# Optimization experiments

Measured on AMD Instinct MI355X. Metric: run time of the kernel, lower is better.

The kernel has to match this reference:

```python
import jax, jax.numpy as jnp
import numpy as np

IMG_H, IMG_W = 256, 704  # full image shape (img_metas['img_shape'])
EPS = 1e-5
B, N_CAM, D_REF, C_CH = 1, 6, 1, 256
HF, WF = 32, 88
DD = 64
BEV_H = BEV_W = 128
Q = BEV_H * BEV_W


def inverse_sigmoid(x, eps=1e-5):
    x = jnp.clip(x, 0.0, 1.0)
    return jnp.log(jnp.clip(x, eps) / jnp.clip(1.0 - x, eps))


def grid_sample_2d(feat, grid):
    # feat [N,C,H,W], grid [N,Hg,Wg,2] (x,y in [-1,1]); bilinear, zeros padding, align_corners=False
    Nn, C, H, W = feat.shape
    x = (grid[..., 0] + 1.0) * 0.5 * W - 0.5
    y = (grid[..., 1] + 1.0) * 0.5 * H - 0.5
    x0 = jnp.floor(x)
    y0 = jnp.floor(y)
    wx = x - x0
    wy = y - y0
    x0 = x0.astype(jnp.int32)
    y0 = y0.astype(jnp.int32)

    def gather(ix, iy):
        valid = (ix >= 0) & (ix < W) & (iy >= 0) & (iy < H)
        ixc = jnp.clip(ix, 0, W - 1)
        iyc = jnp.clip(iy, 0, H - 1)
        v = jax.vmap(lambda f, jx, jy: f[:, jy, jx])(feat, ixc, iyc)  # [N,C,Hg,Wg]
        return v * valid[:, None].astype(feat.dtype)

    return (gather(x0, y0) * ((1 - wx) * (1 - wy))[:, None]
            + gather(x0 + 1, y0) * (wx * (1 - wy))[:, None]
            + gather(x0, y0 + 1) * ((1 - wx) * wy)[:, None]
            + gather(x0 + 1, y0 + 1) * (wx * wy)[:, None])


def grid_sample_3d(vol, grid):
    # vol [N,C,D,H,W], grid [N,Dg,Hg,Wg,3] (x,y,z); trilinear, zeros padding, align_corners=False
    Nn, C, D, H, W = vol.shape
    x = (grid[..., 0] + 1.0) * 0.5 * W - 0.5
    y = (grid[..., 1] + 1.0) * 0.5 * H - 0.5
    z = (grid[..., 2] + 1.0) * 0.5 * D - 0.5
    x0 = jnp.floor(x); y0 = jnp.floor(y); z0 = jnp.floor(z)
    wx = x - x0; wy = y - y0; wz = z - z0
    x0 = x0.astype(jnp.int32); y0 = y0.astype(jnp.int32); z0 = z0.astype(jnp.int32)

    def gather(ix, iy, iz):
        valid = (ix >= 0) & (ix < W) & (iy >= 0) & (iy < H) & (iz >= 0) & (iz < D)
        ixc = jnp.clip(ix, 0, W - 1)
        iyc = jnp.clip(iy, 0, H - 1)
        izc = jnp.clip(iz, 0, D - 1)
        v = jax.vmap(lambda f, jx, jy, jz: f[:, jz, jy, jx])(vol, ixc, iyc, izc)
        return v * valid[:, None].astype(vol.dtype)

    return (gather(x0, y0, z0) * ((1 - wx) * (1 - wy) * (1 - wz))[:, None]
            + gather(x0 + 1, y0, z0) * (wx * (1 - wy) * (1 - wz))[:, None]
            + gather(x0, y0 + 1, z0) * ((1 - wx) * wy * (1 - wz))[:, None]
            + gather(x0 + 1, y0 + 1, z0) * (wx * wy * (1 - wz))[:, None]
            + gather(x0, y0, z0 + 1) * ((1 - wx) * (1 - wy) * wz)[:, None]
            + gather(x0 + 1, y0, z0 + 1) * (wx * (1 - wy) * wz)[:, None]
            + gather(x0, y0 + 1, z0 + 1) * ((1 - wx) * wy * wz)[:, None]
            + gather(x0 + 1, y0 + 1, z0 + 1) * (wx * wy * wz)[:, None])


def setup_inputs() -> dict:
    key = jax.random.key(0)
    ks = jax.random.split(key, 12)
    feat = jax.random.normal(ks[0], (B * N_CAM, C_CH, HF, WF), jnp.float32)
    bev_queries = jax.random.normal(ks[1], (B, Q, C_CH), jnp.float32)
    bev_pos = jax.random.normal(ks[2], (B, Q, C_CH), jnp.float32)
    reference_points = jax.random.uniform(ks[3], (B, D_REF, Q, 3), jnp.float32)
    pc_range = jnp.array([-51.2, -51.2, -5.0, 51.2, 51.2, 3.0], jnp.float32)
    # semi-realistic lidar->image projection matrices: intrinsics * axis-swap * yaw per camera
    f, cx, cy = 500.0, IMG_W / 2.0, IMG_H / 2.0
    K = np.array([[f, 0, cx, 0], [0, f, cy, 0], [0, 0, 1, 0], [0, 0, 0, 1]], np.float32)
    A = np.array([[0, -1, 0, 0], [0, 0, -1, 0], [1, 0, 0, 0], [0, 0, 0, 1]], np.float32)
    mats = []
    for i in range(N_CAM):
        th = 2.0 * np.pi * i / N_CAM
        c, s = np.cos(th), np.sin(th)
        R = np.array([[c, s, 0, 0], [-s, c, 0, 0], [0, 0, 1, 0], [0, 0, 0, 1]], np.float32)
        mats.append(K @ A @ R)
    lidar_to_img = jnp.asarray(np.stack(mats))[None]  # [1,N,4,4]
    depth_prob = jax.random.uniform(ks[4], (B * N_CAM, DD, HF, WF), jnp.float32)
    sc = 0.02
    return {
        'feat': feat, 'bev_queries': bev_queries, 'bev_pos': bev_pos,
        'reference_points': reference_points, 'pc_range': pc_range,
        'lidar_to_img': lidar_to_img, 'depth_prob': depth_prob,
        'w_pos': jax.random.normal(ks[5], (C_CH, 1), jnp.float32) * sc,
        'b_pos': jnp.zeros((1,), jnp.float32),
        'w_img': jax.random.normal(ks[6], (C_CH, N_CAM * 2), jnp.float32) * sc,
        'b_img': jnp.zeros((N_CAM * 2,), jnp.float32),
        'w_att': jax.random.normal(ks[7], (C_CH, N_CAM), jnp.float32) * sc,
        'b_att': jnp.zeros((N_CAM,), jnp.float32),
        'conv_w': jax.random.normal(ks[8], (C_CH, C_CH, 3, 3), jnp.float32) * sc,
        'conv_b': jnp.zeros((C_CH,), jnp.float32),
        'bn_gamma': jnp.ones((C_CH,), jnp.float32),
        'bn_beta': jnp.zeros((C_CH,), jnp.float32),
        'bn_mean': jnp.zeros((C_CH,), jnp.float32),
        'bn_var': jnp.ones((C_CH,), jnp.float32),
        'se_w': jax.random.normal(ks[9], (C_CH, C_CH), jnp.float32) * sc,
        'se_b': jnp.zeros((C_CH,), jnp.float32),
        'cbam_w': jax.random.normal(ks[10], (1, 2, 7, 7), jnp.float32) * 0.05,
        'cbam_b': jnp.zeros((1,), jnp.float32),
        'bev_h': BEV_H, 'bev_w': BEV_W,
    }


def reference(feat, bev_queries, bev_pos, reference_points, pc_range, lidar_to_img, depth_prob,
              w_pos, b_pos, w_img, b_img, w_att, b_att, conv_w, conv_b,
              bn_gamma, bn_beta, bn_mean, bn_var, se_w, se_b, cbam_w, cbam_b, bev_h, bev_w):
    Bq, Qn = bev_queries.shape[:2]
    D = reference_points.shape[1]
    N = lidar_to_img.shape[1]
    BN, C, Hf, Wf = feat.shape
    q = bev_queries + bev_pos
    pos_offset = q @ w_pos + b_pos  # [B,Q,1] (only_use_height)
    z = jax.nn.sigmoid(inverse_sigmoid(reference_points[..., 2:3]) + pos_offset[:, None])
    rp = jnp.concatenate([reference_points[..., :2], z], axis=-1)  # [B,D,Q,3]
    attn = (q @ w_att + b_att).reshape(Bq, 1, Qn, N, 1)
    img_off = q @ w_img + b_img  # [B,Q,2N]
    # unnormalize to lidar coords; apply_3d_transformation == identity (no aug)
    pts = rp * (pc_range[3:] - pc_range[:3]) + pc_range[:3]
    pts4 = jnp.concatenate([pts, jnp.ones_like(pts[..., :1])], axis=-1)  # [B,D,Q,4]
    cam = jnp.einsum('bnij,bdqj->dbnqi', lidar_to_img, pts4)  # [D,B,N,Q,4]
    ref_depth = cam[..., 2:3]
    mask = ref_depth > EPS
    xy = cam[..., :2] / jnp.maximum(cam[..., 2:3], EPS)
    xy = xy / jnp.array([IMG_W, IMG_H], dtype=xy.dtype)
    xy = (xy - 0.5) * 2.0
    mask = mask & (xy[..., 0:1] > -1.0) & (xy[..., 0:1] < 1.0) & (xy[..., 1:2] > -1.0) & (xy[..., 1:2] < 1.0)
    Dd = depth_prob.shape[1]
    ref_depth = (ref_depth / Dd - 0.5) * 2.0
    mask = mask & (ref_depth > -1.0) & (ref_depth < 1.0)
    bev_mask = jnp.transpose(mask, (1, 4, 3, 2, 0)).astype(feat.dtype)  # [B,1,Q,N,D]
    off = img_off.reshape(Bq, Qn, N, 2).transpose(0, 2, 1, 3)[None] / jnp.array([Wf, Hf], dtype=feat.dtype)
    xy = xy + off  # [D,B,N,Q,2]
    grid = xy.transpose(1, 2, 3, 0, 4).reshape(BN, Qn, D, 2)
    sampled = grid_sample_2d(feat, grid).reshape(Bq, N, C, Qn, D).transpose(0, 2, 3, 1, 4)  # [B,C,Q,N,D]
    grid3 = jnp.concatenate([xy, ref_depth], axis=-1).transpose(1, 2, 3, 0, 4).reshape(BN, 1, Qn, D, 3)
    dp = grid_sample_3d(depth_prob[:, None], grid3).reshape(Bq, N, 1, Qn, D).transpose(0, 2, 3, 1, 4)
    bev_mask = jnp.nan_to_num(dp) * bev_mask
    w = jax.nn.sigmoid(attn) * jnp.nan_to_num(bev_mask)
    agg = (jnp.nan_to_num(sampled) * w)[..., 0].sum(-1)  # [B,C,Q] (D==1)
    x = agg.reshape(Bq, C, bev_h, bev_w)
    dn = ('NCHW', 'OIHW', 'NCHW')
    x = jax.lax.conv_general_dilated(x, conv_w, (1, 1), ((1, 1), (1, 1)), dimension_numbers=dn) + conv_b[None, :, None, None]
    x = (x - bn_mean[None, :, None, None]) * (bn_gamma / jnp.sqrt(bn_var + 1e-5))[None, :, None, None] + bn_beta[None, :, None, None]
    x = jax.nn.relu(x)
    s = x.mean(axis=(2, 3))  # SE: global avg pool + 1x1 conv + sigmoid
    x = x * jax.nn.sigmoid(s @ se_w.T + se_b)[:, :, None, None]
    a = jnp.concatenate([x.max(axis=1, keepdims=True), x.mean(axis=1, keepdims=True)], axis=1)  # CBAM spatial
    a = jax.lax.conv_general_dilated(a, cbam_w, (1, 1), ((3, 3), (3, 3)), dimension_numbers=dn) + cbam_b[None, :, None, None]
    x = x * jax.nn.sigmoid(a)
    out = x.reshape(Bq, C, bev_h * bev_w).transpose(0, 2, 1)
    return out, rp
```

## Files before the change

kernel.cpp:

```cpp
#include <hip/hip_runtime.h>
#include <math.h>

#define QN   16384
#define CCH  256
#define NCAM 6
#define HFD  32
#define WFD  88
#define DDD  64
#define BEVH 128
#define BEVW 128
#define IMGW 704.0f
#define IMGH 256.0f
#define EPSV 1e-5f

typedef __attribute__((ext_vector_type(8))) short bf8_t;
typedef __attribute__((ext_vector_type(8))) unsigned short us8;
typedef __attribute__((ext_vector_type(4))) unsigned short us4;
typedef __attribute__((ext_vector_type(4))) float f4_t;

__device__ __forceinline__ float sigmoidf_(float x){ return 1.0f/(1.0f+__expf(-x)); }

__device__ __forceinline__ unsigned short f2bf(float f){
    unsigned int b = __float_as_uint(f);
    b += 0x7FFFu + ((b >> 16) & 1u);
    return (unsigned short)(b >> 16);
}
__device__ __forceinline__ float bf2f(unsigned short u){
    return __uint_as_float(((unsigned int)u) << 16);
}

__global__ __launch_bounds__(256) void k_prep(const float* __restrict__ feat, unsigned short* __restrict__ feat_tH,
                                              const float* __restrict__ cw, unsigned short* __restrict__ wtH,
                                              const float* __restrict__ se_w, float* __restrict__ se_wT,
                                              float* __restrict__ ssum){
    int b = blockIdx.x;
    if (b < 4224){
        __shared__ float tile[32][33];
        int n   = b / 704;
        int rem = b - n*704;
        int cb  = (rem / 88) * 32;
        int pb  = (rem % 88) * 32;
        int tx = threadIdx.x & 31, ty = threadIdx.x >> 5;
        for (int r = ty; r < 32; r += 8)
            tile[r][tx] = feat[(size_t)(n*256 + cb + r)*2816 + pb + tx];
        __syncthreads();
        for (int r = ty; r < 32; r += 8)
            feat_tH[(size_t)(n*2816 + pb + r)*256 + cb + tx] = f2bf(tile[tx][r]);
    } else if (b < 6528){
        int b2 = b - 4224;
        if (b2 == 0) ssum[threadIdx.x] = 0.f;
        int idx = b2*256 + threadIdx.x;
        int ci = idx & 255;
        int co = (idx >> 8) & 255;
        int kk = idx >> 16;
        int kh = kk/3, kw = kk - kh*3;
        int chunk = ci >> 6, ciin = ci & 63;
        size_t dst = ((((size_t)(kh*4 + chunk)*3 + kw)*256 + co) << 6) + ciin;
        wtH[dst] = f2bf(cw[(size_t)(co*256 + ci)*9 + kk]);
    } else {
        __shared__ float tile[32][33];
        int tb = b - 6528;
        int rb_ = (tb >> 3) * 32;
        int cb_ = (tb & 7) * 32;
        int tx = threadIdx.x & 31, ty = threadIdx.x >> 5;
        for (int r = ty; r < 32; r += 8)
            tile[r][tx] = se_w[(size_t)(rb_ + r)*256 + cb_ + tx];
        __syncthreads();
        for (int r = ty; r < 32; r += 8)
            se_wT[(size_t)(cb_ + r)*256 + rb_ + tx] = tile[tx][r];
    }
}

__global__ __launch_bounds__(256) void k_proj(
    const float* __restrict__ bq, const float* __restrict__ bpos,
    const float* __restrict__ refp,
    const float* __restrict__ w_pos, const float* __restrict__ b_pos,
    const float* __restrict__ w_img, const float* __restrict__ w_att,
    float* __restrict__ Sg, float* __restrict__ out_rp)
{
    __shared__ float wlf[19][260];
    __shared__ unsigned short Aq[64][264];
    __shared__ float sl[64][20];
    int tid = threadIdx.x;
    int lane = tid & 63, wid = tid >> 6;
    int l15 = lane & 15, quad = lane >> 4;
    int q0 = blockIdx.x * 64;

    wlf[0][tid] = w_pos[tid];
    #pragma unroll
    for (int r = 0; r < 6; r++){
        int idx = r*256 + tid;
        int c = idx / 6, j = idx - 6*c;
        wlf[1 + j][c] = w_att[idx];
    }
    #pragma unroll
    for (int r = 0; r < 12; r++){
        int idx = r*256 + tid;
        int c = idx / 12, j = idx - 12*c;
        wlf[7 + j][c] = w_img[idx];
    }
    #pragma unroll
    for (int r = 0; r < 16; r++){
        int row = r*4 + wid;
        int cc  = lane * 4;
        float4 a = *(const float4*)(bq   + (size_t)(q0+row)*CCH + cc);
        float4 b = *(const float4*)(bpos + (size_t)(q0+row)*CCH + cc);
        us4 o;
        o.x = f2bf(a.x+b.x); o.y = f2bf(a.y+b.y); o.z = f2bf(a.z+b.z); o.w = f2bf(a.w+b.w);
        *(us4*)&Aq[row][cc] = o;
    }
    __syncthreads();

    f4_t acc0 = (f4_t){0.f,0.f,0.f,0.f};
    f4_t acc1 = (f4_t){0.f,0.f,0.f,0.f};
    #pragma unroll
    for (int kc = 0; kc < 8; kc++){
        bf8_t af = *(bf8_t*)&Aq[wid*16 + l15][kc*32 + quad*8];
        bf8_t b0, b1;
        {
            const float* wr = &wlf[l15][kc*32 + quad*8];
            float4 w0 = *(const float4*)wr;
            float4 w1 = *(const float4*)(wr + 4);
            b0[0]=(short)f2bf(w0.x); b0[1]=(short)f2bf(w0.y); b0[2]=(short)f2bf(w0.z); b0[3]=(short)f2bf(w0.w);
            b0[4]=(short)f2bf(w1.x); b0[5]=(short)f2bf(w1.y); b0[6]=(short)f2bf(w1.z); b0[7]=(short)f2bf(w1.w);
        }
        if (l15 < 3){
            const float* wr = &wlf[16 + l15][kc*32 + quad*8];
            float4 w0 = *(const float4*)wr;
            float4 w1 = *(const float4*)(wr + 4);
            b1[0]=(short)f2bf(w0.x); b1[1]=(short)f2bf(w0.y); b1[2]=(short)f2bf(w0.z); b1[3]=(short)f2bf(w0.w);
            b1[4]=(short)f2bf(w1.x); b1[5]=(short)f2bf(w1.y); b1[6]=(short)f2bf(w1.z); b1[7]=(short)f2bf(w1.w);
        } else {
            b1 = (bf8_t){0,0,0,0,0,0,0,0};
        }
        acc0 = __builtin_amdgcn_mfma_f32_16x16x32_bf16(af, b0, acc0, 0, 0, 0);
        acc1 = __builtin_amdgcn_mfma_f32_16x16x32_bf16(af, b1, acc1, 0, 0, 0);
    }
    #pragma unroll
    for (int r = 0; r < 4; r++){
        int qq = wid*16 + quad*4 + r;
        sl[qq][l15] = acc0[r];
        if (l15 < 3) sl[qq][16 + l15] = acc1[r];
    }
    __syncthreads();

    if (tid < 64){
        int q = q0 + tid;
        float pos_off = sl[tid][0] + b_pos[0];
        float rx = refp[q*3+0], ry = refp[q*3+1], rz = refp[q*3+2];
        float zc_ = fminf(fmaxf(rz, 0.f), 1.f);
        float inv = logf(fmaxf(zc_, EPSV) / fmaxf(1.f - zc_, EPSV));
        float znew = sigmoidf_(inv + pos_off);
        out_rp[q*3+0] = rx; out_rp[q*3+1] = ry; out_rp[q*3+2] = znew;
        sl[tid][19] = znew;
    }
    __syncthreads();

    for (int i = tid; i < 64*20; i += 256)
        Sg[(size_t)q0*20 + i] = ((const float*)sl)[i];
}

__global__ __launch_bounds__(256) void k_geomagg(
    const float* __restrict__ refp, const float* __restrict__ pcr,
    const float* __restrict__ l2i, const float* __restrict__ dpr,
    const float* __restrict__ b_img, const float* __restrict__ b_att,
    const float* __restrict__ Sg, const unsigned short* __restrict__ feat_tH,
    unsigned short* __restrict__ aggH)
{
    __shared__ float sgl[8][20];
    __shared__ int   so_l[192];
    __shared__ float sw_l[192];
    int q0 = blockIdx.x * 8;
    int tid = threadIdx.x;
    int wid = tid >> 6, lane = tid & 63;

    if (tid < 160) ((float*)sgl)[tid] = Sg[(size_t)q0*20 + tid];
    __syncthreads();

    {
        int sub = lane >> 5;
        int n   = lane & 31;
        if (n < NCAM){
            int ql = wid*2 + sub;
            int q  = q0 + ql;
            float att  = sgl[ql][1+n] + b_att[n];
            float offx = (sgl[ql][7+2*n] + b_img[2*n])   / (float)WFD;
            float offy = (sgl[ql][8+2*n] + b_img[2*n+1]) / (float)HFD;
            float znew = sgl[ql][19];
            float rx = refp[q*3+0], ry = refp[q*3+1];
            float lo0=pcr[0], lo1=pcr[1], lo2=pcr[2];
            float hi0=pcr[3], hi1=pcr[4], hi2=pcr[5];
            float px = rx*(hi0-lo0)+lo0, py = ry*(hi1-lo1)+lo1, pz = znew*(hi2-lo2)+lo2;
            const float* M = l2i + n*16;
            float cx = M[0]*px + M[1]*py + M[2]*pz  + M[3];
            float cy = M[4]*px + M[5]*py + M[6]*pz  + M[7];
            float cz = M[8]*px + M[9]*py + M[10]*pz + M[11];
            bool m = cz > EPSV;
            float zdiv = fmaxf(cz, EPSV);
            float u = (cx/zdiv)/IMGW; u = (u - 0.5f)*2.f;
            float v = (cy/zdiv)/IMGH; v = (v - 0.5f)*2.f;
            m = m && (u > -1.f) && (u < 1.f) && (v > -1.f) && (v < 1.f);
            float rdn = (cz/(float)DDD - 0.5f)*2.f;
            m = m && (rdn > -1.f) && (rdn < 1.f);

            int base = ql*24 + n*4;
            float wq = 0.f, xs = 0.f, ys = 0.f;
            if (m){
                float u2 = u + offx, v2 = v + offy;
                xs = (u2 + 1.f)*0.5f*WFD - 0.5f;
                ys = (v2 + 1.f)*0.5f*HFD - 0.5f;
                float zs = (rdn + 1.f)*0.5f*DDD - 0.5f;
                float fx = floorf(xs), fy = floorf(ys), fz = floorf(zs);
                int x0=(int)fx, y0=(int)fy, z0=(int)fz;
                float wx = xs-fx, wy = ys-fy, wz = zs-fz;
                float dp = 0.f;
                const float* vol = dpr + (size_t)n*DDD*HFD*WFD;
                #pragma unroll
                for (int dz=0; dz<2; dz++)
                #pragma unroll
                for (int dy=0; dy<2; dy++)
                #pragma unroll
                for (int dx=0; dx<2; dx++){
                    int ix=x0+dx, iy=y0+dy, iz=z0+dz;
                    if (ix>=0 && ix<WFD && iy>=0 && iy<HFD && iz>=0 && iz<DDD){
                        float ww = (dx?wx:1.f-wx)*(dy?wy:1.f-wy)*(dz?wz:1.f-wz);
                        dp += ww * vol[(size_t)(iz*HFD+iy)*WFD + ix];
                    }
                }
                wq = sigmoidf_(att) * dp;
            }
            if (m && wq != 0.f){
                float fx = floorf(xs), fy = floorf(ys);
                int x0=(int)fx, y0=(int)fy;
                float wx = xs-fx, wy = ys-fy;
                float cwv[4] = {(1.f-wx)*(1.f-wy), wx*(1.f-wy), (1.f-wx)*wy, wx*wy};
                int xi[4] = {x0, x0+1, x0, x0+1};
                int yi[4] = {y0, y0, y0+1, y0+1};
                #pragma unroll
                for (int k=0;k<4;k++){
                    bool ok = (xi[k]>=0 && xi[k]<WFD && yi[k]>=0 && yi[k]<HFD);
                    so_l[base+k] = ok ? ((n*HFD + yi[k])*WFD + xi[k]) : 0;
                    sw_l[base+k] = ok ? wq*cwv[k] : 0.f;
                }
            } else {
                #pragma unroll
                for (int k=0;k<4;k++){ so_l[base+k] = 0; sw_l[base+k] = 0.f; }
            }
        }
    }
    __syncthreads();

    {
        int half = lane >> 5, li = lane & 31;
        int c8 = li * 8;
        int ql = wid*2 + half;
        float a[8] = {0.f,0.f,0.f,0.f,0.f,0.f,0.f,0.f};
        #pragma unroll
        for (int k=0;k<24;k++){
            float w = sw_l[ql*24+k];
            us8 v = *(const us8*)(feat_tH + (size_t)so_l[ql*24+k]*CCH + c8);
            #pragma unroll
            for (int j=0;j<8;j++) a[j] += w * bf2f((unsigned short)v[j]);
        }
        us8 o;
        #pragma unroll
        for (int j=0;j<8;j++) o[j] = f2bf(a[j]);
        *(us8*)(aggH + (size_t)(q0+ql)*CCH + c8) = o;
    }
}

__global__ __launch_bounds__(256, 3) void k_conv2(const unsigned short* __restrict__ aggH,
    const unsigned short* __restrict__ wtH, const float* __restrict__ conv_b,
    const float* __restrict__ bn_g, const float* __restrict__ bn_b,
    const float* __restrict__ bn_m, const float* __restrict__ bn_v,
    float* __restrict__ xN, float* __restrict__ ssum)
{
    __shared__ unsigned short Al[130][72];
    __shared__ unsigned short Bl[3][64][72];
    __shared__ float sacc[64];

    int h   = blockIdx.x;
    int co0 = blockIdx.y * 64;
    int tid  = threadIdx.x;
    int lane = tid & 63, wid = tid >> 6;
    int m_q = (wid & 1) * 64;
    int n_q = (wid >> 1) * 32;
    int l15 = lane & 15, quad = lane >> 4;

    f4_t acc[4][2];
    #pragma unroll
    for (int i=0;i<4;i++)
    #pragma unroll
    for (int j=0;j<2;j++) acc[i][j] = (f4_t){0.f,0.f,0.f,0.f};

    int arow = tid >> 1;
    int aseg = (tid & 1) * 32;

    if (tid < 16){
        int r = (tid >> 3) ? 129 : 0;
        int sg = (tid & 7) * 8;
        *(us8*)&Al[r][sg] = (us8){0,0,0,0,0,0,0,0};
    }
    if (tid < 64) sacc[tid] = 0.f;

    us8 ra[4], rb[3][2];
    const us8 z8 = (us8){0,0,0,0,0,0,0,0};

    #define LOADSTAGE(s) { \
        int kh_ = (s) >> 2; \
        int ph_ = h + kh_ - 1; \
        if (ph_ >= 0 && ph_ < BEVH){ \
            const unsigned short* ap_ = aggH + ((size_t)(ph_*BEVW + arow)*CCH + (((s) & 3) << 6) + aseg); \
            ra[0] = *(const us8*)ap_;        ra[1] = *(const us8*)(ap_ + 8); \
            ra[2] = *(const us8*)(ap_ + 16); ra[3] = *(const us8*)(ap_ + 24); \
        } else { ra[0]=z8; ra[1]=z8; ra[2]=z8; ra[3]=z8; } \
        const unsigned short* bp_ = wtH + (size_t)(s)*49152 + (size_t)co0*64; \
        _Pragma("unroll") \
        for (int kw_=0; kw_<3; kw_++){ \
            _Pragma("unroll") \
            for (int j_=0; j_<2; j_++) \
                rb[kw_][j_] = *(const us8*)(bp_ + kw_*16384 + (j_*256 + tid)*8); \
        } \
    }

    LOADSTAGE(0);
    for (int s=0; s<12; s++){
        __syncthreads();
        *(us8*)&Al[arow+1][aseg]      = ra[0];
        *(us8*)&Al[arow+1][aseg+8]    = ra[1];
        *(us8*)&Al[arow+1][aseg+16]   = ra[2];
        *(us8*)&Al[arow+1][aseg+24]   = ra[3];
        {
            int bco = tid >> 3;
            int ciin = (tid & 7) * 8;
            #pragma unroll
            for (int kw_=0; kw_<3; kw_++){
                #pragma unroll
                for (int j_=0; j_<2; j_++)
                    *(us8*)&Bl[kw_][j_*32 + bco][ciin] = rb[kw_][j_];
            }
        }
        __syncthreads();
        if (s < 11) LOADSTAGE(s+1);
        #pragma unroll
        for (int ks=0; ks<2; ks++){
            #pragma unroll
            for (int kw=0; kw<3; kw++){
                bf8_t af[4], bfr[2];
                #pragma unroll
                for (int i=0;i<4;i++) af[i]  = *(bf8_t*)&Al[m_q + i*16 + l15 + kw][ks*32 + quad*8];
                #pragma unroll
                for (int j=0;j<2;j++) bfr[j] = *(bf8_t*)&Bl[kw][n_q + j*16 + l15][ks*32 + quad*8];
                #pragma unroll
                for (int i=0;i<4;i++)
                #pragma unroll
                for (int j=0;j<2;j++)
                    acc[i][j] = __builtin_amdgcn_mfma_f32_16x16x32_bf16(af[i], bfr[j], acc[i][j], 0, 0, 0);
            }
        }
    }
    #undef LOADSTAGE

    #pragma unroll
    for (int j=0;j<2;j++){
        int col = n_q + j*16 + l15;
        int co = co0 + col;
        float sc = bn_g[co] * rsqrtf(bn_v[co] + 1e-5f);
        float sh = bn_b[co] - bn_m[co]*sc;
        float cb = conv_b[co];
        float part = 0.f;
        #pragma unroll
        for (int i=0;i<4;i++){
            #pragma unroll
            for (int r=0;r<4;r++){
                int m = m_q + i*16 + quad*4 + r;
                int p = h*BEVW + m;
                float y = fmaxf((acc[i][j][r] + cb)*sc + sh, 0.f);
                xN[(size_t)p*CCH + co] = y;
                part += y;
            }
        }
        atomicAdd(&sacc[col], part);
    }
    __syncthreads();
    if (tid < 64) atomicAdd(&ssum[co0 + tid], sacc[tid]);
}

__global__ __launch_bounds__(256) void k_maps2(const float* __restrict__ xN,
    const float* __restrict__ ssum, const float* __restrict__ se_wT, const float* __restrict__ se_b,
    float* __restrict__ scale_g, float* __restrict__ amax, float* __restrict__ amean)
{
    __shared__ float smv[256];
    __shared__ float scl[256];
    int t = threadIdx.x;
    smv[t] = ssum[t] * (1.f/16384.f);
    __syncthreads();
    float a0=0.f, a1=0.f, a2=0.f, a3=0.f;
    for (int k=0; k<256; k+=4){
        a0 += smv[k]   * se_wT[(size_t)(k  )*256 + t];
        a1 += smv[k+1] * se_wT[(size_t)(k+1)*256 + t];
        a2 += smv[k+2] * se_wT[(size_t)(k+2)*256 + t];
        a3 += smv[k+3] * se_wT[(size_t)(k+3)*256 + t];
    }
    float sv = sigmoidf_(se_b[t] + ((a0+a1)+(a2+a3)));
    scl[t] = sv;
    if (blockIdx.x == 0) scale_g[t] = sv;
    __syncthreads();

    int wid = t >> 6, lane = t & 63;
    int p0 = blockIdx.x * 64;
    float4 sc = *(const float4*)&scl[lane*4];
    for (int i=0; i<16; i++){
        int p = p0 + i*4 + wid;
        float4 v = *(const float4*)&xN[(size_t)p*CCH + lane*4];
        float a = v.x*sc.x, b = v.y*sc.y, c = v.z*sc.z, d = v.w*sc.w;
        float mx = fmaxf(fmaxf(a,b), fmaxf(c,d));
        float sm = a+b+c+d;
        #pragma unroll
        for (int off=1; off<64; off<<=1){
            mx = fmaxf(mx, __shfl_xor(mx, off, 64));
            sm += __shfl_xor(sm, off, 64);
        }
        if (lane == 0){ amax[p] = mx; amean[p] = sm*(1.f/256.f); }
    }
}

__global__ __launch_bounds__(256) void k_final2(const float* __restrict__ xN,
    const float* __restrict__ scale_g, const float* __restrict__ amax, const float* __restrict__ amean,
    const float* __restrict__ cw, const float* __restrict__ cb, float* __restrict__ out)
{
    __shared__ float am2[7][128];
    __shared__ float av2[7][128];
    __shared__ float wcb[98];
    __shared__ float scl[256];
    __shared__ float amap_l[64];

    int b = blockIdx.x;
    int h  = b >> 1;
    int w0 = (b & 1) * 64;
    int t = threadIdx.x;

    scl[t] = scale_g[t];
    if (t < 98) wcb[t] = cw[t];
    for (int idx = t; idx < 896; idx += 256){
        int r = idx >> 7, c = idx & 127;
        int ph = h + r - 3;
        bool ok = (ph >= 0 && ph < BEVH);
        am2[r][c] = ok ? amax[ph*BEVW + c] : 0.f;
        av2[r][c] = ok ? amean[ph*BEVW + c] : 0.f;
    }
    __syncthreads();

    if (t < 64){
        int px = w0 + t;
        float acc = cb[0];
        #pragma unroll
        for (int kh=0; kh<7; kh++){
            #pragma unroll
            for (int kw=0; kw<7; kw++){
                int pw = px + kw - 3;
                if (pw >= 0 && pw < BEVW)
                    acc += am2[kh][pw]*wcb[kh*7+kw] + av2[kh][pw]*wcb[49 + kh*7+kw];
            }
        }
        amap_l[t] = sigmoidf_(acc);
    }
    __syncthreads();

    int lane = t & 63, sub = t >> 6;
    int c4 = lane * 4;
    float4 sc = *(const float4*)&scl[c4];
    for (int i=0; i<16; i++){
        int pxl = sub*16 + i;
        int p = h*BEVW + w0 + pxl;
        float am = amap_l[pxl];
        float4 v = *(const float4*)&xN[(size_t)p*CCH + c4];
        float4 o;
        o.x = v.x*sc.x*am; o.y = v.y*sc.y*am; o.z = v.z*sc.z*am; o.w = v.w*sc.w*am;
        *(float4*)&out[(size_t)p*CCH + c4] = o;
    }
}

extern "C" void kernel_launch(void* const* d_in, const int* in_sizes, int n_in,
                              void* d_out, int out_size, void* d_ws, size_t ws_size,
                              hipStream_t stream) {
    const float* feat   = (const float*)d_in[0];
    const float* bq     = (const float*)d_in[1];
    const float* bpos   = (const float*)d_in[2];
    const float* refp   = (const float*)d_in[3];
    const float* pcr    = (const float*)d_in[4];
    const float* l2i    = (const float*)d_in[5];
    const float* dpr    = (const float*)d_in[6];
    const float* w_pos  = (const float*)d_in[7];
    const float* b_pos  = (const float*)d_in[8];
    const float* w_img  = (const float*)d_in[9];
    const float* b_img  = (const float*)d_in[10];
    const float* w_att  = (const float*)d_in[11];
    const float* b_att  = (const float*)d_in[12];
    const float* conv_w = (const float*)d_in[13];
    const float* conv_b = (const float*)d_in[14];
    const float* bn_g   = (const float*)d_in[15];
    const float* bn_b   = (const float*)d_in[16];
    const float* bn_m   = (const float*)d_in[17];
    const float* bn_v   = (const float*)d_in[18];
    const float* se_w   = (const float*)d_in[19];
    const float* se_b   = (const float*)d_in[20];
    const float* cbw    = (const float*)d_in[21];
    const float* cbb    = (const float*)d_in[22];
    float* out = (float*)d_out;

    float* ws = (float*)d_ws;
    size_t o = 0;
    unsigned short* feat_tH = (unsigned short*)(ws + o); o += (size_t)6*2816*128;
    unsigned short* wtH  = (unsigned short*)(ws + o); o += (size_t)9*256*128;
    unsigned short* aggH = (unsigned short*)(ws + o); o += (size_t)QN*128;
    float* xN      = ws + o;  o += (size_t)QN*256;
    float* se_wT   = ws + o;  o += (size_t)256*256;
    float* Sg      = ws + o;  o += (size_t)QN*20;
    float* ssum    = ws + o;  o += 256;
    float* scale_g = ws + o;  o += 256;
    float* amax    = ws + o;  o += QN;
    float* amean   = ws + o;  o += QN;

    k_prep<<<6592, 256, 0, stream>>>(feat, feat_tH, conv_w, wtH, se_w, se_wT, ssum);
    k_proj<<<256, 256, 0, stream>>>(bq, bpos, refp, w_pos, b_pos, w_img, w_att,
                                    Sg, out + (size_t)QN*256);
    k_geomagg<<<2048, 256, 0, stream>>>(refp, pcr, l2i, dpr, b_img, b_att,
                                        Sg, feat_tH, aggH);
    k_conv2<<<dim3(128,4), 256, 0, stream>>>(aggH, wtH, conv_b, bn_g, bn_b, bn_m, bn_v, xN, ssum);
    k_maps2<<<256, 256, 0, stream>>>(xN, ssum, se_wT, se_b, scale_g, amax, amean);
    k_final2<<<256, 256, 0, stream>>>(xN, scale_g, amax, amean, cbw, cbb, out);
}
```

Measured before the change: 219.1 us.

## Split K across warps in conv GEMM with LDS reduction and padded rows

```diff
diff --git a/kernel.cpp b/kernel.cpp
--- a/kernel.cpp
+++ b/kernel.cpp
@@ -275,23 +275,26 @@
     const float* __restrict__ bn_m, const float* __restrict__ bn_v,
     float* __restrict__ xN, float* __restrict__ ssum)
 {
-    __shared__ unsigned short Al[130][72];
-    __shared__ unsigned short Bl[3][64][72];
+    __shared__ __align__(16) char smem[48944];
+    unsigned short (*Al)[76]     = (unsigned short (*)[76])smem;
+    unsigned short (*Bl)[64][76] = (unsigned short (*)[64][76])(smem + 19760);
     __shared__ float sacc[64];
 
     int h   = blockIdx.x;
     int co0 = blockIdx.y * 64;
     int tid  = threadIdx.x;
     int lane = tid & 63, wid = tid >> 6;
-    int m_q = (wid & 1) * 64;
-    int n_q = (wid >> 1) * 32;
+    int mh  = wid & 1;
+    int ksw = wid >> 1;
+    int m_q = mh * 64;
+    int kbase = ksw * 32;
     int l15 = lane & 15, quad = lane >> 4;
 
-    f4_t acc[4][2];
+    f4_t acc[4][4];
     #pragma unroll
     for (int i=0;i<4;i++)
     #pragma unroll
-    for (int j=0;j<2;j++) acc[i][j] = (f4_t){0.f,0.f,0.f,0.f};
+    for (int j=0;j<4;j++) acc[i][j] = (f4_t){0.f,0.f,0.f,0.f};
 
     int arow = tid >> 1;
     int aseg = (tid & 1) * 32;
@@ -343,44 +346,62 @@
         __syncthreads();
         if (s < 11) LOADSTAGE(s+1);
         #pragma unroll
-        for (int ks=0; ks<2; ks++){
-            #pragma unroll
-            for (int kw=0; kw<3; kw++){
-                bf8_t af[4], bfr[2];
-                #pragma unroll
-                for (int i=0;i<4;i++) af[i]  = *(bf8_t*)&Al[m_q + i*16 + l15 + kw][ks*32 + quad*8];
-                #pragma unroll
-                for (int j=0;j<2;j++) bfr[j] = *(bf8_t*)&Bl[kw][n_q + j*16 + l15][ks*32 + quad*8];
-                #pragma unroll
-                for (int i=0;i<4;i++)
-                #pragma unroll
-                for (int j=0;j<2;j++)
-                    acc[i][j] = __builtin_amdgcn_mfma_f32_16x16x32_bf16(af[i], bfr[j], acc[i][j], 0, 0, 0);
+        for (int kw=0; kw<3; kw++){
+            bf8_t af[4], bfr[4];
+            #pragma unroll
+            for (int i=0;i<4;i++) af[i]  = *(bf8_t*)&Al[m_q + i*16 + l15 + kw][kbase + quad*8];
+            #pragma unroll
+            for (int j=0;j<4;j++) bfr[j] = *(bf8_t*)&Bl[kw][j*16 + l15][kbase + quad*8];
+            #pragma unroll
+            for (int i=0;i<4;i++)
+            #pragma unroll
+            for (int j=0;j<4;j++)
+                acc[i][j] = __builtin_amdgcn_mfma_f32_16x16x32_bf16(af[i], bfr[j], acc[i][j], 0, 0, 0);
+        }
+    }
+    #undef LOADSTAGE
+
+    __syncthreads();
+    float (*red)[64][68] = (float (*)[64][68])smem;
+    if (ksw == 1){
+        #pragma unroll
+        for (int j=0;j<4;j++)
+        #pragma unroll
+        for (int i=0;i<4;i++)
+            *(f4_t*)&red[mh][j*16 + l15][i*16 + quad*4] = acc[i][j];
+    }
+    __syncthreads();
+
+    if (ksw == 0){
+        #pragma unroll
+        for (int j=0;j<4;j++)
+        #pragma unroll
+        for (int i=0;i<4;i++){
+            f4_t o = *(const f4_t*)&red[mh][j*16 + l15][i*16 + quad*4];
+            acc[i][j][0] += o[0]; acc[i][j][1] += o[1];
+            acc[i][j][2] += o[2]; acc[i][j][3] += o[3];
+        }
+        #pragma unroll
+        for (int j=0;j<4;j++){
+            int col = j*16 + l15;
+            int co = co0 + col;
+            float sc = bn_g[co] * rsqrtf(bn_v[co] + 1e-5f);
+            float sh = bn_b[co] - bn_m[co]*sc;
+            float cb = conv_b[co];
+            float part = 0.f;
+            #pragma unroll
+            for (int i=0;i<4;i++){
+                #pragma unroll
+                for (int r=0;r<4;r++){
+                    int m = m_q + i*16 + quad*4 + r;
+                    int p = h*BEVW + m;
+                    float y = fmaxf((acc[i][j][r] + cb)*sc + sh, 0.f);
+                    xN[(size_t)p*CCH + co] = y;
+                    part += y;
+                }
             }
-        }
-    }
-    #undef LOADSTAGE
-
-    #pragma unroll
-    for (int j=0;j<2;j++){
-        int col = n_q + j*16 + l15;
-        int co = co0 + col;
-        float sc = bn_g[co] * rsqrtf(bn_v[co] + 1e-5f);
-        float sh = bn_b[co] - bn_m[co]*sc;
-        float cb = conv_b[co];
-        float part = 0.f;
-        #pragma unroll
-        for (int i=0;i<4;i++){
-            #pragma unroll
-            for (int r=0;r<4;r++){
-                int m = m_q + i*16 + quad*4 + r;
-                int p = h*BEVW + m;
-                float y = fmaxf((acc[i][j][r] + cb)*sc + sh, 0.f);
-                xN[(size_t)p*CCH + co] = y;
-                part += y;
-            }
-        }
-        atomicAdd(&sacc[col], part);
+            atomicAdd(&sacc[col], part);
+        }
     }
     __syncthreads();
     if (tid < 64) atomicAdd(&ssum[co0 + tid], sacc[tid]);
```

Result: slower. 280.9 us (+28.2%).
